# Optimization experiments

Hardware: AMD Instinct MI355X
Metric: run time of the kernel (lower is better)

## Reference

```python
import jax, jax.numpy as jnp
import numpy as np

B, M, N, K = 8192, 512, 2048, 16
P = 50      # top-k support size per iteration
EPS = 0.01


def soft_threshold(x, theta, p):
    # x: [B, N]
    if p == 0:
        return jnp.sign(x) * jax.nn.relu(jnp.abs(x) - theta)
    abs_ = jnp.abs(x)
    topk_vals, _ = jax.lax.top_k(abs_, p)          # sorted descending
    thresh = topk_vals[:, -1]                      # min of top-k, per row
    keep = (abs_ > thresh[:, None]).astype(x.dtype)
    shrunk = jnp.sign(x) * jax.nn.relu(abs_ - theta)
    return keep * x + (1.0 - keep) * shrunk


def setup_inputs() -> dict:
    key = jax.random.key(0)
    k_y, k_A = jax.random.split(key)
    y = jax.random.normal(k_y, (B, M), dtype=jnp.float32)
    A = jax.random.normal(k_A, (M, N), dtype=jnp.float32) / np.sqrt(M)
    gamma = jnp.full((K,), 3.0, dtype=jnp.float32)
    theta = jnp.full((K,), 0.02, dtype=jnp.float32)
    a_param = jnp.full((K,), 0.01, dtype=jnp.float32)
    v = jnp.ones((K,), dtype=jnp.float32)
    vu = jnp.full((K,), 0.05, dtype=jnp.float32)
    theta_init = jnp.float32(1.0)
    return {"y": y, "A": A, "gamma": gamma, "theta": theta,
            "a_param": a_param, "v": v, "vu": vu,
            "theta_init": theta_init, "info": 0}


def reference(y, A, gamma, theta, a_param, v, vu, theta_init, info):
    # forward_op(x)  = x @ A.T   : [B,N] -> [B,M]
    # backward_op(b) = b @ A     : [B,M] -> [B,N]
    x = jnp.zeros((y.shape[0], A.shape[1]), dtype=y.dtype)
    for i in range(K):
        t = theta_init if i == 0 else theta[i]
        gain = 1.0 + t * vu[i] * jnp.exp(-v[i] * jnp.abs(x))
        b = (gain * x) @ A.T - y                 # residual in measurement space
        c = b @ A                                # gradient step direction
        x_new = soft_threshold(x - gamma[i] * c, theta[i], P)
        overshoot = 1.0 + a_param[i] / (jnp.abs(x_new - x) + EPS)
        x = overshoot * x_new + (1.0 - overshoot) * x
    return (x, jnp.zeros((K, 1), dtype=y.dtype), jnp.zeros((K, 1), dtype=y.dtype))
```

## Files before the change

### kernel.cpp

```cpp
#include <hip/hip_runtime.h>
#include <math.h>

#define Bsz  8192
#define Mdim 512
#define Ndim 2048
#define Kit  16
#define Pk   50
#define EPSv 0.01f

typedef __attribute__((ext_vector_type(8))) short bf16x8;
typedef __attribute__((ext_vector_type(4))) float f32x4;

static __device__ __forceinline__ unsigned short f2bf(float f) {
    unsigned u = __float_as_uint(f);
    return (unsigned short)((u + 0x7fffu + ((u >> 16) & 1u)) >> 16);
}
static __device__ __forceinline__ float bf2f(unsigned short h) {
    return __uint_as_float(((unsigned)h) << 16);
}

static __device__ __forceinline__ void gl16(const void* g, void* l) {
    __builtin_amdgcn_global_load_lds(
        (const __attribute__((address_space(1))) unsigned int*)g,
        (__attribute__((address_space(3))) unsigned int*)l, 16, 0, 0);
}

#define PIPE_BARRIER() __builtin_amdgcn_s_barrier()

#define MFMA3(acc_, bh_, bl_, ah_, al_)                                           \
    do {                                                                          \
        acc_ = __builtin_amdgcn_mfma_f32_16x16x32_bf16(bh_, ah_, acc_, 0, 0, 0);  \
        acc_ = __builtin_amdgcn_mfma_f32_16x16x32_bf16(bh_, al_, acc_, 0, 0, 0);  \
        acc_ = __builtin_amdgcn_mfma_f32_16x16x32_bf16(bl_, ah_, acc_, 0, 0, 0);  \
    } while (0)

__global__ __launch_bounds__(256) void presplit_A(
    const float* __restrict__ A, unsigned short* __restrict__ Ah,
    unsigned short* __restrict__ Al, unsigned short* __restrict__ AhT,
    unsigned short* __restrict__ AlT)
{
    int idx = blockIdx.x * 256 + threadIdx.x;
    int m = idx >> 11, n = idx & (Ndim - 1);
    float a = A[idx];
    unsigned short h = f2bf(a);
    unsigned short l = f2bf(a - bf2f(h));
    Ah[idx] = h; Al[idx] = l;
    AhT[(size_t)n * Mdim + m] = h;
    AlT[(size_t)n * Mdim + m] = l;
}

__global__ __launch_bounds__(256) void split_negy_kernel(const float* __restrict__ y,
                                                         unsigned short* __restrict__ bS) {
    int i = blockIdx.x * 256 + threadIdx.x;
    float4 v = ((const float4*)y)[i];
    int idx = i * 4;
    int r = idx >> 9, c = idx & 511;
    float f0 = -v.x, f1 = -v.y, f2 = -v.z, f3 = -v.w;
    unsigned short h0 = f2bf(f0), h1 = f2bf(f1), h2 = f2bf(f2), h3 = f2bf(f3);
    ushort4 hv = make_ushort4(h0, h1, h2, h3);
    ushort4 lv = make_ushort4(f2bf(f0 - bf2f(h0)), f2bf(f1 - bf2f(h1)),
                              f2bf(f2 - bf2f(h2)), f2bf(f3 - bf2f(h3)));
    *(ushort4*)(bS + (size_t)r * 1024 + c)       = hv;
    *(ushort4*)(bS + (size_t)r * 1024 + 512 + c) = lv;
}

__global__ __launch_bounds__(512, 2) void gemm1_mfma(
    const unsigned short* __restrict__ zS,
    const unsigned short* __restrict__ Ah, const unsigned short* __restrict__ Al,
    const float* __restrict__ y, unsigned short* __restrict__ bS)
{
    enum { NT = 32 };
    const int tid  = threadIdx.x;
    const int lane = tid & 63, w = tid >> 6;
    const int lm   = lane & 15, quad = lane >> 4;
    const int g    = w >> 2;
    const int wg   = w & 3;
    const int wrow = (wg >> 1) * 64;
    const int wcol = (wg & 1) * 64;

    int d   = blockIdx.y * gridDim.x + blockIdx.x;
    int sid = (d & 7) * 32 + (d >> 3);
    const int m0 = (sid & 3) * 128, r0 = (sid >> 2) * 128;

    __shared__ __attribute__((aligned(16))) unsigned short smem[2 * 32768];

    f32x4 acc[4][4];
#pragma unroll
    for (int i = 0; i < 4; i++)
#pragma unroll
        for (int j = 0; j < 4; j++) acc[i][j] = (f32x4)0.f;

    const unsigned short *zhp[2], *zlp[2], *ahp[2], *alp[2]; int doff[2];
#pragma unroll
    for (int s = 0; s < 2; s++) {
        int off = ((wg * 2 + s) << 10) + lane * 16;
        int row = off >> 6;
        int kb  = (off & 63) ^ (((row >> 1) & 3) << 4);
        doff[s] = (wg * 2 + s) << 10;
        int kbase = g * 1024 + (kb >> 1);
        zhp[s]  = zS + (size_t)(r0 + row) * 4096 + kbase;
        zlp[s]  = zS + (size_t)(r0 + row) * 4096 + 2048 + kbase;
        ahp[s]  = Ah + (size_t)(m0 + row) * 2048 + kbase;
        alp[s]  = Al + (size_t)(m0 + row) * 2048 + kbase;
    }

    const int X   = ((lm >> 1) & 3) << 4;
    const int cbx = (quad * 16) ^ X;

    auto STAGE = [&](int t) {
        char* base = (char*)smem + (t & 1) * 65536 + g * 32768;
        const int ko = t * 32;
#pragma unroll
        for (int s = 0; s < 2; s++) {
            gl16(zhp[s] + ko, base +     0 + doff[s]);
            gl16(zlp[s] + ko, base +  8192 + doff[s]);
            gl16(ahp[s] + ko, base + 16384 + doff[s]);
            gl16(alp[s] + ko, base + 24576 + doff[s]);
        }
    };

    auto BUF = [&](int t) -> const char* {
        return (const char*)smem + (t & 1) * 65536 + g * 32768;
    };
    auto LD_FULL = [&](const char* B0, bf16x8 (&zh)[4], bf16x8 (&zl)[4],
                       bf16x8 (&ah)[4], bf16x8 (&al)[4]) {
        const char* zhB = B0, *zlB = B0 + 8192;
        const char* ahB = B0 + 16384, *alB = B0 + 24576;
#pragma unroll
        for (int fi = 0; fi < 4; fi++) {
            int zr = wrow + fi * 16 + lm;
            zh[fi] = *(const bf16x8*)(zhB + zr * 64 + cbx);
            zl[fi] = *(const bf16x8*)(zlB + zr * 64 + cbx);
        }
#pragma unroll
        for (int fj = 0; fj < 4; fj++) {
            int ar = wcol + fj * 16 + lm;
            ah[fj] = *(const bf16x8*)(ahB + ar * 64 + cbx);
            al[fj] = *(const bf16x8*)(alB + ar * 64 + cbx);
        }
    };

    bf16x8 zhA[4], zlA[4], ahA[4], alA[4];
    bf16x8 zhB[4], zlB[4], ahB[4], alB[4];

    STAGE(0);
    asm volatile("s_waitcnt vmcnt(0)" ::: "memory");
    PIPE_BARRIER();
    STAGE(1);
    LD_FULL(BUF(0), zhA, zlA, ahA, alA);

    auto STEP = [&](int t,
                    bf16x8 (&czh)[4], bf16x8 (&czl)[4], bf16x8 (&cah)[4], bf16x8 (&cal)[4],
                    bf16x8 (&nzh)[4], bf16x8 (&nzl)[4], bf16x8 (&nah)[4], bf16x8 (&nal)[4]) {
        asm volatile("s_waitcnt lgkmcnt(0)" ::: "memory");
        asm volatile("s_waitcnt vmcnt(0)" ::: "memory");
        PIPE_BARRIER();
        if (t + 2 < NT) STAGE(t + 2);
        if (t + 1 < NT) LD_FULL(BUF(t + 1), nzh, nzl, nah, nal);
        __builtin_amdgcn_sched_barrier(0);
        __builtin_amdgcn_s_setprio(1);
#pragma unroll
        for (int fi = 0; fi < 4; fi++) {
#pragma unroll
            for (int fj = 0; fj < 4; fj++) {
                MFMA3(acc[fi][fj], czh[fi], czl[fi], cah[fj], cal[fj]);
            }
        }
        __builtin_amdgcn_s_setprio(0);
        __builtin_amdgcn_sched_barrier(0);
    };

    for (int t = 0; t < NT; t += 2) {
        STEP(t,     zhA, zlA, ahA, alA, zhB, zlB, ahB, alB);
        STEP(t + 1, zhB, zlB, ahB, alB, zhA, zlA, ahA, alA);
    }

    float* cmb = (float*)smem;
    __syncthreads();
    if (g == 1) {
#pragma unroll
        for (int fi = 0; fi < 4; fi++)
#pragma unroll
            for (int fj = 0; fj < 4; fj++)
#pragma unroll
                for (int r = 0; r < 4; r++) {
                    int row = wrow + fi * 16 + quad * 4 + r;
                    int col = wcol + fj * 16 + lm;
                    cmb[row * 132 + col] = acc[fi][fj][r];
                }
    }
    __syncthreads();
    if (g == 0) {
#pragma unroll
        for (int fi = 0; fi < 4; fi++)
#pragma unroll
            for (int fj = 0; fj < 4; fj++)
#pragma unroll
                for (int r = 0; r < 4; r++) {
                    int row = wrow + fi * 16 + quad * 4 + r;
                    int col = wcol + fj * 16 + lm;
                    float bv = acc[fi][fj][r] + cmb[row * 132 + col]
                             - y[(size_t)(r0 + row) * Mdim + (m0 + col)];
                    unsigned short h = f2bf(bv);
                    bS[(size_t)(r0 + row) * 1024 + (m0 + col)]       = h;
                    bS[(size_t)(r0 + row) * 1024 + 512 + (m0 + col)] = f2bf(bv - bf2f(h));
                }
    }
}

__global__ __launch_bounds__(512, 2) void gemm2_mfma(
    const unsigned short* __restrict__ bS,
    const unsigned short* __restrict__ AhT, const unsigned short* __restrict__ AlT,
    float* __restrict__ c)
{
    enum { NT = 16 };
    const int tid  = threadIdx.x;
    const int lane = tid & 63, w = tid >> 6;
    const int lm   = lane & 15, quad = lane >> 4;
    const int wrow = (w >> 2) * 128;
    const int wcol = (w & 3) * 64;

    int d   = blockIdx.y * gridDim.x + blockIdx.x;
    int sid = (d & 7) * 32 + (d >> 3);
    const int n0 = (sid & 7) * 256, r0 = (sid >> 3) * 256;

    __shared__ __attribute__((aligned(16))) unsigned short smem[2 * 32768];

    f32x4 acc[8][4];
#pragma unroll
    for (int i = 0; i < 8; i++)
#pragma unroll
        for (int j = 0; j < 4; j++) acc[i][j] = (f32x4)0.f;

    const unsigned short *bhp[2], *blp[2], *ahp[2], *alp[2]; int doff[2];
#pragma unroll
    for (int s = 0; s < 2; s++) {
        int off = ((w * 2 + s) << 10) + lane * 16;
        int row = off >> 6;
        int kb  = (off & 63) ^ (((row >> 1) & 3) << 4);
        doff[s] = (w * 2 + s) << 10;
        bhp[s]  = bS  + (size_t)(r0 + row) * 1024 + (kb >> 1);
        blp[s]  = bS  + (size_t)(r0 + row) * 1024 + 512 + (kb >> 1);
        ahp[s]  = AhT + (size_t)(n0 + row) * 512 + (kb >> 1);
        alp[s]  = AlT + (size_t)(n0 + row) * 512 + (kb >> 1);
    }

    const int X   = ((lm >> 1) & 3) << 4;
    const int cbx = (quad * 16) ^ X;

    auto STAGE = [&](int t) {
        char* base = (char*)smem + (t & 1) * 65536;
        const int ko = t * 32;
#pragma unroll
        for (int s = 0; s < 2; s++) {
            gl16(bhp[s] + ko, base +     0 + doff[s]);
            gl16(blp[s] + ko, base + 16384 + doff[s]);
            gl16(ahp[s] + ko, base + 32768 + doff[s]);
            gl16(alp[s] + ko, base + 49152 + doff[s]);
        }
    };

    auto BUF = [&](int t) -> const char* {
        return (const char*)smem + (t & 1) * 65536;
    };
    auto LD_A = [&](const char* B0, bf16x8 (&ah)[4], bf16x8 (&al)[4]) {
        const char* ahB = B0 + 32768; const char* alB = B0 + 49152;
#pragma unroll
        for (int fj = 0; fj < 4; fj++) {
            int ar = wcol + fj * 16 + lm;
            ah[fj] = *(const bf16x8*)(ahB + ar * 64 + cbx);
            al[fj] = *(const bf16x8*)(alB + ar * 64 + cbx);
        }
    };
    auto LD_B = [&](const char* B0, int rbase, bf16x8 (&bh)[4], bf16x8 (&bl)[4]) {
        const char* bhB = B0; const char* blB = B0 + 16384;
#pragma unroll
        for (int fi = 0; fi < 4; fi++) {
            int br = wrow + (rbase + fi) * 16 + lm;
            bh[fi] = *(const bf16x8*)(bhB + br * 64 + cbx);
            bl[fi] = *(const bf16x8*)(blB + br * 64 + cbx);
        }
    };

    bf16x8 ahf[4], alf[4], b03h[4], b03l[4], b47h[4], b47l[4];

    STAGE(0);
    asm volatile("s_waitcnt vmcnt(0)" ::: "memory");
    PIPE_BARRIER();
    LD_B(BUF(0), 0, b03h, b03l);

    for (int t = 0; t < NT; ++t) {
        const char* B0 = BUF(t);
        if (t + 1 < NT) STAGE(t + 1);
        LD_A(B0, ahf, alf);
        LD_B(B0, 4, b47h, b47l);
        __builtin_amdgcn_sched_barrier(0);
        __builtin_amdgcn_s_setprio(1);
#pragma unroll
        for (int fi = 0; fi < 4; fi++) {
#pragma unroll
            for (int fj = 0; fj < 4; fj++) {
                MFMA3(acc[fi][fj], b03h[fi], b03l[fi], ahf[fj], alf[fj]);
            }
        }
        __builtin_amdgcn_s_setprio(0);
        __builtin_amdgcn_sched_barrier(0);
        asm volatile("s_waitcnt vmcnt(0)" ::: "memory");
        PIPE_BARRIER();
        if (t + 1 < NT) LD_B(BUF(t + 1), 0, b03h, b03l);
        __builtin_amdgcn_sched_barrier(0);
        __builtin_amdgcn_s_setprio(1);
#pragma unroll
        for (int fi = 0; fi < 4; fi++) {
#pragma unroll
            for (int fj = 0; fj < 4; fj++) {
                MFMA3(acc[fi + 4][fj], b47h[fi], b47l[fi], ahf[fj], alf[fj]);
            }
        }
        __builtin_amdgcn_s_setprio(0);
        __builtin_amdgcn_sched_barrier(0);
    }

#pragma unroll
    for (int fi = 0; fi < 8; fi++)
#pragma unroll
        for (int fj = 0; fj < 4; fj++)
#pragma unroll
            for (int r = 0; r < 4; r++) {
                int row = r0 + wrow + fi * 16 + quad * 4 + r;
                int col = n0 + wcol + fj * 16 + lm;
                c[(size_t)row * Ndim + col] = acc[fi][fj][r];
            }
}

__global__ __launch_bounds__(256) void topk_update_kernel(
    float* __restrict__ uz, float* __restrict__ x,
    const float* __restrict__ gamma, const float* __restrict__ theta,
    const float* __restrict__ a_param, const float* __restrict__ vv,
    const float* __restrict__ vu, int it)
{
    const int row = blockIdx.x;
    const int t   = threadIdx.x;
    float* crow = uz + (size_t)row * Ndim;
    float* xrow = x  + (size_t)row * Ndim;
    const float g = gamma[it];

    float4 c0 = *(const float4*)(crow + 4 * t);
    float4 c1 = *(const float4*)(crow + 4 * t + 1024);
    float4 x0 = *(const float4*)(xrow + 4 * t);
    float4 x1 = *(const float4*)(xrow + 4 * t + 1024);
    float cv[8] = { c0.x, c0.y, c0.z, c0.w, c1.x, c1.y, c1.z, c1.w };
    float xv[8] = { x0.x, x0.y, x0.z, x0.w, x1.x, x1.y, x1.z, x1.w };

    float uvals[8];
    unsigned keys[8];
#pragma unroll
    for (int e = 0; e < 8; e++) {
        uvals[e] = xv[e] - g * cv[e];
        keys[e]  = __float_as_uint(fabsf(uvals[e]));
    }

    __shared__ unsigned bins[2048];
    __shared__ unsigned sel[2];
    __shared__ unsigned wsum[4];

    unsigned prefix = 0;
    unsigned k = Pk;
#pragma unroll
    for (int pass = 0; pass < 3; ++pass) {
        const int      shift  = (pass == 0) ? 20 : (pass == 1) ? 9 : 0;
        const unsigned cmask  = (pass == 2) ? 511u : 2047u;
        const unsigned himask = (pass == 0) ? 0u
                              : (pass == 1) ? (0xFFFFFFFFu << 20)
                                            : (0xFFFFFFFFu << 9);
        uint4 zz = { 0u, 0u, 0u, 0u };
        ((uint4*)bins)[t]       = zz;
        ((uint4*)bins)[t + 256] = zz;
        __syncthreads();
#pragma unroll
        for (int e = 0; e < 8; e++) {
            if ((keys[e] & himask) == prefix)
                atomicAdd(&bins[(keys[e] >> shift) & cmask], 1u);
        }
        __syncthreads();
        const int base = 2040 - 8 * t;
        uint4 q0 = *(const uint4*)&bins[base];
        uint4 q1 = *(const uint4*)&bins[base + 4];
        unsigned s  = q0.x + q0.y + q0.z + q0.w + q1.x + q1.y + q1.z + q1.w;
        unsigned sc = s;
        const int ln = t & 63;
#pragma unroll
        for (int off = 1; off < 64; off <<= 1) {
            unsigned o = __shfl_up(sc, (unsigned)off);
            if (ln >= off) sc += o;
        }
        if (ln == 63) wsum[t >> 6] = sc;
        __syncthreads();
        unsigned wpre = 0;
#pragma unroll
        for (int ww = 0; ww < 3; ww++)
            if (ww < (t >> 6)) wpre += wsum[ww];
        unsigned pre = wpre + sc - s;
        if (pre < k && pre + s >= k) {
            unsigned vals[8] = { q1.w, q1.z, q1.y, q1.x, q0.w, q0.z, q0.y, q0.x };
            unsigned p2 = pre;
#pragma unroll
            for (int j = 0; j < 8; j++) {
                unsigned cb = vals[j];
                if (p2 < k && p2 + cb >= k) { sel[0] = (unsigned)(base + 7 - j); sel[1] = k - p2; }
                p2 += cb;
            }
        }
        __syncthreads();
        prefix |= sel[0] << shift;
        k = sel[1];
    }
    const float thresh = __uint_as_float(prefix);

    const float th = theta[it];
    const float ap = a_param[it];
    const bool haveNext = (it + 1) < Kit;
    float tn = 0.f, vn = 0.f, vun = 0.f;
    if (haveNext) { tn = theta[it + 1]; vn = vv[it + 1]; vun = vu[it + 1]; }

    float xo[8];
    unsigned short zh8[8], zl8[8];
#pragma unroll
    for (int e = 0; e < 8; e++) {
        float uval = uvals[e];
        float au   = fabsf(uval);
        bool keep  = au > thresh;
        float shr  = copysignf(fmaxf(au - th, 0.f), uval);
        float xn   = keep ? uval : shr;
        float dlt  = xn - xv[e];
        float ov   = 1.f + ap / (fabsf(dlt) + EPSv);
        float xr   = xv[e] + ov * dlt;
        xo[e] = xr;
        float z = (1.f + tn * vun * __expf(-vn * fabsf(xr))) * xr;
        unsigned short h = f2bf(z);
        zh8[e] = h;
        zl8[e] = f2bf(z - bf2f(h));
    }
    float4 a0 = { xo[0], xo[1], xo[2], xo[3] };
    float4 a1 = { xo[4], xo[5], xo[6], xo[7] };
    *(float4*)(xrow + 4 * t) = a0;
    *(float4*)(xrow + 4 * t + 1024) = a1;
    if (haveNext) {
        unsigned short* zp = (unsigned short*)crow;
        *(ushort4*)(zp + 4 * t)        = make_ushort4(zh8[0], zh8[1], zh8[2], zh8[3]);
        *(ushort4*)(zp + 1024 + 4 * t) = make_ushort4(zh8[4], zh8[5], zh8[6], zh8[7]);
        *(ushort4*)(zp + 2048 + 4 * t) = make_ushort4(zl8[0], zl8[1], zl8[2], zl8[3]);
        *(ushort4*)(zp + 3072 + 4 * t) = make_ushort4(zl8[4], zl8[5], zl8[6], zl8[7]);
    }
}

extern "C" void kernel_launch(void* const* d_in, const int* in_sizes, int n_in,
                              void* d_out, int out_size, void* d_ws, size_t ws_size,
                              hipStream_t stream) {
    const float* y       = (const float*)d_in[0];
    const float* A       = (const float*)d_in[1];
    const float* gamma   = (const float*)d_in[2];
    const float* theta   = (const float*)d_in[3];
    const float* a_param = (const float*)d_in[4];
    const float* v       = (const float*)d_in[5];
    const float* vu      = (const float*)d_in[6];

    float* x = (float*)d_out;

    char* ws = (char*)d_ws;
    float*          uz = (float*)ws;
    unsigned short* bS = (unsigned short*)(ws + (size_t)Bsz * Ndim * 4);
    unsigned short* Ah = (unsigned short*)(ws + (size_t)80 * 1024 * 1024);
    unsigned short* Al  = Ah  + (size_t)Mdim * Ndim;
    unsigned short* AhT = Al  + (size_t)Mdim * Ndim;
    unsigned short* AlT = AhT + (size_t)Mdim * Ndim;

    hipMemsetAsync(d_out, 0, (size_t)out_size * sizeof(float), stream);

    dim3 g1(Mdim / 128, Bsz / 128);
    dim3 g2(Ndim / 256, Bsz / 256);

    presplit_A<<<(Mdim * Ndim) / 256, dim3(256), 0, stream>>>(A, Ah, Al, AhT, AlT);
    split_negy_kernel<<<(Bsz * Mdim / 4) / 256, dim3(256), 0, stream>>>(y, bS);

    for (int it = 0; it < Kit; ++it) {
        if (it > 0)
            gemm1_mfma<<<g1, dim3(512), 0, stream>>>((const unsigned short*)uz, Ah, Al, y, bS);
        gemm2_mfma<<<g2, dim3(512), 0, stream>>>(bS, AhT, AlT, uz);
        topk_update_kernel<<<Bsz, dim3(256), 0, stream>>>(uz, x, gamma, theta, a_param, v, vu, it);
    }
}
```

Measured before the change: 2.305 ms.

## Drop split-K in gemm1, use 128x64 tiles with 256-thread blocks

Gemm1 loses its two-group split-K (512 threads, 128x128 tile, LDS reduction) and becomes a single 4-wave block that walks the full K=2048 over a 128x64 output tile, with twice as many blocks. The aim is to remove the cross-group LDS combine and its barriers, shrink shared memory per block so more blocks can be resident, and give better grid coverage. The cost is less A-operand reuse per block, since the z tile is reloaded for each 64-column slice, and a longer serial K loop per block.

```diff
diff --git a/kernel.cpp b/kernel.cpp
--- a/kernel.cpp
+++ b/kernel.cpp
@@ -64,94 +64,95 @@
     *(ushort4*)(bS + (size_t)r * 1024 + 512 + c) = lv;
 }
 
-__global__ __launch_bounds__(512, 2) void gemm1_mfma(
+__global__ __launch_bounds__(256, 2) void gemm1_mfma(
     const unsigned short* __restrict__ zS,
     const unsigned short* __restrict__ Ah, const unsigned short* __restrict__ Al,
     const float* __restrict__ y, unsigned short* __restrict__ bS)
 {
-    enum { NT = 32 };
+    enum { NT = 64 };
     const int tid  = threadIdx.x;
     const int lane = tid & 63, w = tid >> 6;
     const int lm   = lane & 15, quad = lane >> 4;
-    const int g    = w >> 2;
-    const int wg   = w & 3;
-    const int wrow = (wg >> 1) * 64;
-    const int wcol = (wg & 1) * 64;
+    const int wrow = (w >> 1) * 64;
+    const int wcol = (w & 1) * 32;
 
     int d   = blockIdx.y * gridDim.x + blockIdx.x;
-    int sid = (d & 7) * 32 + (d >> 3);
-    const int m0 = (sid & 3) * 128, r0 = (sid >> 2) * 128;
-
-    __shared__ __attribute__((aligned(16))) unsigned short smem[2 * 32768];
-
-    f32x4 acc[4][4];
+    int sid = (d & 7) * 64 + (d >> 3);
+    const int m0 = (sid & 7) * 64, r0 = (sid >> 3) * 128;
+
+    __shared__ __attribute__((aligned(16))) unsigned short smem[2 * 12288];
+
+    f32x4 acc[4][2];
 #pragma unroll
     for (int i = 0; i < 4; i++)
 #pragma unroll
-        for (int j = 0; j < 4; j++) acc[i][j] = (f32x4)0.f;
-
-    const unsigned short *zhp[2], *zlp[2], *ahp[2], *alp[2]; int doff[2];
+        for (int j = 0; j < 2; j++) acc[i][j] = (f32x4)0.f;
+
+    const unsigned short *zhp[2], *zlp[2]; int zoff[2];
 #pragma unroll
     for (int s = 0; s < 2; s++) {
-        int off = ((wg * 2 + s) << 10) + lane * 16;
+        int off = ((w * 2 + s) << 10) + lane * 16;
         int row = off >> 6;
         int kb  = (off & 63) ^ (((row >> 1) & 3) << 4);
-        doff[s] = (wg * 2 + s) << 10;
-        int kbase = g * 1024 + (kb >> 1);
-        zhp[s]  = zS + (size_t)(r0 + row) * 4096 + kbase;
-        zlp[s]  = zS + (size_t)(r0 + row) * 4096 + 2048 + kbase;
-        ahp[s]  = Ah + (size_t)(m0 + row) * 2048 + kbase;
-        alp[s]  = Al + (size_t)(m0 + row) * 2048 + kbase;
+        zoff[s] = (w * 2 + s) << 10;
+        zhp[s]  = zS + (size_t)(r0 + row) * 4096 + (kb >> 1);
+        zlp[s]  = zS + (size_t)(r0 + row) * 4096 + 2048 + (kb >> 1);
+    }
+    const unsigned short *ahp, *alp; int aoff;
+    {
+        int off = (w << 10) + lane * 16;
+        int row = off >> 6;
+        int kb  = (off & 63) ^ (((row >> 1) & 3) << 4);
+        aoff = w << 10;
+        ahp  = Ah + (size_t)(m0 + row) * 2048 + (kb >> 1);
+        alp  = Al + (size_t)(m0 + row) * 2048 + (kb >> 1);
     }
 
     const int X   = ((lm >> 1) & 3) << 4;
     const int cbx = (quad * 16) ^ X;
 
     auto STAGE = [&](int t) {
-        char* base = (char*)smem + (t & 1) * 65536 + g * 32768;
+        char* base = (char*)smem + (t & 1) * 24576;
         const int ko = t * 32;
 #pragma unroll
         for (int s = 0; s < 2; s++) {
-            gl16(zhp[s] + ko, base +     0 + doff[s]);
-            gl16(zlp[s] + ko, base +  8192 + doff[s]);
-            gl16(ahp[s] + ko, base + 16384 + doff[s]);
-            gl16(alp[s] + ko, base + 24576 + doff[s]);
-        }
-    };
-
+            gl16(zhp[s] + ko, base +    0 + zoff[s]);
+            gl16(zlp[s] + ko, base + 8192 + zoff[s]);
+        }
+        gl16(ahp + ko, base + 16384 + aoff);
+        gl16(alp + ko, base + 20480 + aoff);
+    };
     auto BUF = [&](int t) -> const char* {
-        return (const char*)smem + (t & 1) * 65536 + g * 32768;
+        return (const char*)smem + (t & 1) * 24576;
     };
     auto LD_FULL = [&](const char* B0, bf16x8 (&zh)[4], bf16x8 (&zl)[4],
-                       bf16x8 (&ah)[4], bf16x8 (&al)[4]) {
-        const char* zhB = B0, *zlB = B0 + 8192;
-        const char* ahB = B0 + 16384, *alB = B0 + 24576;
+                       bf16x8 (&ah)[2], bf16x8 (&al)[2]) {
 #pragma unroll
         for (int fi = 0; fi < 4; fi++) {
             int zr = wrow + fi * 16 + lm;
-            zh[fi] = *(const bf16x8*)(zhB + zr * 64 + cbx);
-            zl[fi] = *(const bf16x8*)(zlB + zr * 64 + cbx);
-        }
-#pragma unroll
-        for (int fj = 0; fj < 4; fj++) {
+            zh[fi] = *(const bf16x8*)(B0 +    0 + zr * 64 + cbx);
+            zl[fi] = *(const bf16x8*)(B0 + 8192 + zr * 64 + cbx);
+        }
+#pragma unroll
+        for (int fj = 0; fj < 2; fj++) {
             int ar = wcol + fj * 16 + lm;
-            ah[fj] = *(const bf16x8*)(ahB + ar * 64 + cbx);
-            al[fj] = *(const bf16x8*)(alB + ar * 64 + cbx);
-        }
-    };
-
-    bf16x8 zhA[4], zlA[4], ahA[4], alA[4];
-    bf16x8 zhB[4], zlB[4], ahB[4], alB[4];
+            ah[fj] = *(const bf16x8*)(B0 + 16384 + ar * 64 + cbx);
+            al[fj] = *(const bf16x8*)(B0 + 20480 + ar * 64 + cbx);
+        }
+    };
+
+    bf16x8 zhE[4], zlE[4], ahE[2], alE[2];
+    bf16x8 zhO[4], zlO[4], ahO[2], alO[2];
 
     STAGE(0);
     asm volatile("s_waitcnt vmcnt(0)" ::: "memory");
     PIPE_BARRIER();
+    LD_FULL(BUF(0), zhE, zlE, ahE, alE);
     STAGE(1);
-    LD_FULL(BUF(0), zhA, zlA, ahA, alA);
 
     auto STEP = [&](int t,
-                    bf16x8 (&czh)[4], bf16x8 (&czl)[4], bf16x8 (&cah)[4], bf16x8 (&cal)[4],
-                    bf16x8 (&nzh)[4], bf16x8 (&nzl)[4], bf16x8 (&nah)[4], bf16x8 (&nal)[4]) {
+                    bf16x8 (&czh)[4], bf16x8 (&czl)[4], bf16x8 (&cah)[2], bf16x8 (&cal)[2],
+                    bf16x8 (&nzh)[4], bf16x8 (&nzl)[4], bf16x8 (&nah)[2], bf16x8 (&nal)[2]) {
         asm volatile("s_waitcnt lgkmcnt(0)" ::: "memory");
         asm volatile("s_waitcnt vmcnt(0)" ::: "memory");
         PIPE_BARRIER();
@@ -162,7 +163,7 @@
 #pragma unroll
         for (int fi = 0; fi < 4; fi++) {
 #pragma unroll
-            for (int fj = 0; fj < 4; fj++) {
+            for (int fj = 0; fj < 2; fj++) {
                 MFMA3(acc[fi][fj], czh[fi], czl[fi], cah[fj], cal[fj]);
             }
         }
@@ -171,41 +172,23 @@
     };
 
     for (int t = 0; t < NT; t += 2) {
-        STEP(t,     zhA, zlA, ahA, alA, zhB, zlB, ahB, alB);
-        STEP(t + 1, zhB, zlB, ahB, alB, zhA, zlA, ahA, alA);
-    }
-
-    float* cmb = (float*)smem;
-    __syncthreads();
-    if (g == 1) {
-#pragma unroll
-        for (int fi = 0; fi < 4; fi++)
-#pragma unroll
-            for (int fj = 0; fj < 4; fj++)
-#pragma unroll
-                for (int r = 0; r < 4; r++) {
-                    int row = wrow + fi * 16 + quad * 4 + r;
-                    int col = wcol + fj * 16 + lm;
-                    cmb[row * 132 + col] = acc[fi][fj][r];
-                }
-    }
-    __syncthreads();
-    if (g == 0) {
-#pragma unroll
-        for (int fi = 0; fi < 4; fi++)
-#pragma unroll
-            for (int fj = 0; fj < 4; fj++)
-#pragma unroll
-                for (int r = 0; r < 4; r++) {
-                    int row = wrow + fi * 16 + quad * 4 + r;
-                    int col = wcol + fj * 16 + lm;
-                    float bv = acc[fi][fj][r] + cmb[row * 132 + col]
-                             - y[(size_t)(r0 + row) * Mdim + (m0 + col)];
-                    unsigned short h = f2bf(bv);
-                    bS[(size_t)(r0 + row) * 1024 + (m0 + col)]       = h;
-                    bS[(size_t)(r0 + row) * 1024 + 512 + (m0 + col)] = f2bf(bv - bf2f(h));
-                }
-    }
+        STEP(t,     zhE, zlE, ahE, alE, zhO, zlO, ahO, alO);
+        STEP(t + 1, zhO, zlO, ahO, alO, zhE, zlE, ahE, alE);
+    }
+
+#pragma unroll
+    for (int fi = 0; fi < 4; fi++)
+#pragma unroll
+        for (int fj = 0; fj < 2; fj++)
+#pragma unroll
+            for (int r = 0; r < 4; r++) {
+                int row = r0 + wrow + fi * 16 + quad * 4 + r;
+                int col = m0 + wcol + fj * 16 + lm;
+                float bv = acc[fi][fj][r] - y[(size_t)row * Mdim + col];
+                unsigned short h = f2bf(bv);
+                bS[(size_t)row * 1024 + col]       = h;
+                bS[(size_t)row * 1024 + 512 + col] = f2bf(bv - bf2f(h));
+            }
 }
 
 __global__ __launch_bounds__(512, 2) void gemm2_mfma(
@@ -477,7 +460,7 @@
 
     hipMemsetAsync(d_out, 0, (size_t)out_size * sizeof(float), stream);
 
-    dim3 g1(Mdim / 128, Bsz / 128);
+    dim3 g1(Mdim / 64, Bsz / 128);
     dim3 g2(Ndim / 256, Bsz / 256);
 
     presplit_A<<<(Mdim * Ndim) / 256, dim3(256), 0, stream>>>(A, Ah, Al, AhT, AlT);
@@ -485,7 +468,7 @@
 
     for (int it = 0; it < Kit; ++it) {
         if (it > 0)
-            gemm1_mfma<<<g1, dim3(512), 0, stream>>>((const unsigned short*)uz, Ah, Al, y, bS);
+            gemm1_mfma<<<g1, dim3(256), 0, stream>>>((const unsigned short*)uz, Ah, Al, y, bS);
         gemm2_mfma<<<g2, dim3(512), 0, stream>>>(bS, AhT, AlT, uz);
         topk_update_kernel<<<Bsz, dim3(256), 0, stream>>>(uz, x, gamma, theta, a_param, v, vu, it);
     }
```

Result: slower. 2.454 ms (+6.5%).
